# Kernel optimization log

Hardware: AMD Instinct MI355X
Metric: run time of the kernel (lower is better)

## Reference

```python
import jax, jax.numpy as jnp
import numpy as np

EPS = 1e-5
INF = 1e5


def setup_inputs() -> dict:
    key = jax.random.key(0)
    ks = iter(jax.random.split(key, 32))
    B, N, F, H, NH, C = 2, 384, 64, 64, 4, 32
    def lin(k, fi, fo):
        return jax.random.normal(k, (fi, fo), jnp.float32) / np.sqrt(fi).astype(np.float32)
    d = {}
    d['h'] = jax.random.normal(next(ks), (B, N, F), jnp.float32)
    d['x'] = jax.random.normal(next(ks), (B, N, 3), jnp.float32)
    # edge_model (ConcatenationFilter): Linear(2F+1,H), SiLU, Linear(H,H), SiLU
    d['We0'] = lin(next(ks), 2 * F + 1, H); d['be0'] = jnp.zeros(H, jnp.float32)
    d['We1'] = lin(next(ks), H, H);         d['be1'] = jnp.zeros(H, jnp.float32)
    # semantic_attention_mlp: Linear(H, n_heads), LeakyReLU(0.2)
    d['Ws'] = lin(next(ks), H, NH);         d['bs'] = jnp.zeros(NH, jnp.float32)
    # coefficients_mlp: Linear(H,H), SiLU, Linear(H,C)
    d['Wc0'] = lin(next(ks), H, H);         d['bc0'] = jnp.zeros(H, jnp.float32)
    d['Wc1'] = lin(next(ks), H, C);         d['bc1'] = jnp.zeros(C, jnp.float32)
    # post_norm_mlp: Linear(C,H), SiLU, Linear(H,H)
    d['Wp0'] = lin(next(ks), C, H);         d['bp0'] = jnp.zeros(H, jnp.float32)
    d['Wp1'] = lin(next(ks), H, H);         d['bp1'] = jnp.zeros(H, jnp.float32)
    # coordinate_mlp: Linear(H,H), SiLU, Linear(H,1,bias=False) init gain 1e-3
    d['Wx0'] = lin(next(ks), H, H);         d['bx0'] = jnp.zeros(H, jnp.float32)
    d['Wx1'] = lin(next(ks), H, 1) * 1e-3
    # node_mlp: Linear(NH*H + H + F, H), SiLU, Linear(H, F)
    d['Wn0'] = lin(next(ks), NH * H + H + F, H); d['bn0'] = jnp.zeros(H, jnp.float32)
    d['Wn1'] = lin(next(ks), H, F);         d['bn1'] = jnp.zeros(F, jnp.float32)
    d['log_gamma'] = jnp.zeros(NH, jnp.float32)
    return d


def _forward(h, x, We0, be0, We1, be1, Ws, bs, Wc0, bc0, Wc1, bc1,
             Wp0, bp0, Wp1, bp1, Wx0, bx0, Wx1, Wn0, bn0, Wn1, bn1, log_gamma):
    B, N, F = h.shape
    silu = jax.nn.silu

    # pairwise displacements and distances: (B,N,N,3), (B,N,N,1)
    x_minus_xt = x[:, :, None, :] - x[:, None, :, :]
    norm = jnp.sqrt(jnp.sum(x_minus_xt * x_minus_xt, axis=-1, keepdims=True) + EPS)

    # pairwise node-feature concat + distance -> edge MLP (ConcatenationFilter)
    hi = jnp.broadcast_to(h[:, :, None, :], (B, N, N, F))
    hj = jnp.broadcast_to(h[:, None, :, :], (B, N, N, F))
    e_in = jnp.concatenate([hi, hj, norm], axis=-1)           # (B,N,N,2F+1)
    h_e = silu(silu(e_in @ We0 + be0) @ We1 + be1)            # (B,N,N,H)

    eye = jnp.eye(N, dtype=h.dtype)[None, :, :, None]         # mask self-edges

    # euclidean attention per head, softmax over neighbors j (axis=-2)
    eu = jax.nn.softmax(-(norm + INF * eye) * jnp.exp(log_gamma), axis=-2)  # (B,N,N,NH)
    # semantic attention
    sem_logits = jax.nn.leaky_relu(h_e @ Ws + bs, 0.2) - INF * eye
    sem = jax.nn.softmax(sem_logits, axis=-2)                 # (B,N,N,NH)
    comb = eu * sem
    comb = comb / (jnp.sum(comb, axis=-2, keepdims=True) + EPS)

    # attention-weighted multi-head edge features, aggregated over neighbors
    h_e_att = (comb[..., :, None] * h_e[..., None, :]).reshape(B, N, N, -1)  # (B,N,N,NH*H)
    h_e_agg = jnp.sum(h_e_att, axis=-2)                       # (B,N,NH*H)

    # spatial attention: equivariant combinations of unit direction vectors
    coeff = silu(h_e @ Wc0 + bc0) @ Wc1 + bc1                 # (B,N,N,C)
    x_hat = x_minus_xt / (norm + EPS)                         # (B,N,N,3)
    combinations = coeff[..., :, None] * x_hat[..., None, :]  # (B,N,N,C,3)
    comb_sum = jnp.mean(combinations, axis=2)                 # mean over j -> (B,N,C,3)
    comb_norm = jnp.sum(comb_sum * comb_sum, axis=-1)         # (B,N,C)
    h_comb = silu(comb_norm @ Wp0 + bp0) @ Wp1 + bp1          # (B,N,H)

    # node update (residual)
    node_in = jnp.concatenate([h, h_e_agg, h_comb], axis=-1)
    h_out = h + (silu(node_in @ Wn0 + bn0) @ Wn1 + bn1)

    # coordinate update: scalar-gated displacements, mean over neighbors
    scale = silu(h_e @ Wx0 + bx0) @ Wx1                       # (B,N,N,1)
    x_out = x + jnp.mean(x_minus_xt * scale, axis=2)          # (B,N,3)
    return h_out, x_out


def reference(h, x, We0, be0, We1, be1, Ws, bs, Wc0, bc0, Wc1, bc1,
              Wp0, bp0, Wp1, bp1, Wx0, bx0, Wx1, Wn0, bn0, Wn1, bn1, log_gamma):
    return _forward(h, x, We0, be0, We1, be1, Ws, bs, Wc0, bc0, Wc1, bc1,
                    Wp0, bp0, Wp1, bp1, Wx0, bx0, Wx1, Wn0, bn0, Wn1, bn1, log_gamma)
```

## Files before the change

### kernel.cpp

```cpp
#include <hip/hip_runtime.h>

#define NPT 384
#define NB 2
#define NROW (NB*NPT)
#define NT 6
#define HOFF 49152
#define RECB 1024
#define REC_OFF 424960

typedef unsigned short u16;
typedef unsigned int u32;
typedef __bf16 bf16x8 __attribute__((ext_vector_type(8)));
typedef float f32x4 __attribute__((ext_vector_type(4)));

struct alignas(16) U4 { u32 x, y, z, w; };

constexpr float kEPS = 1e-5f;
constexpr float kINF = 1e5f;

#define WAVE_LDS_FENCE() asm volatile("s_waitcnt lgkmcnt(0)" ::: "memory")

__device__ __forceinline__ u16 f2b(float f) { __bf16 b = (__bf16)f; return __builtin_bit_cast(u16, b); }
__device__ __forceinline__ u32 pk2(float lo, float hi) { return (u32)f2b(lo) | ((u32)f2b(hi) << 16); }
__device__ __forceinline__ float b2f(u32 u) { return __uint_as_float(u << 16); }
__device__ __forceinline__ float silu_f(float v) { return v * __builtin_amdgcn_rcpf(1.f + __expf(-v)); }

__global__ __launch_bounds__(64) void sake_prep(
    const float* __restrict__ h, const float* __restrict__ We0,
    const float* __restrict__ be0, const float* __restrict__ We1,
    const float* __restrict__ Wc0, const float* __restrict__ Wc1,
    const float* __restrict__ Wx0, const float* __restrict__ Ws,
    float* __restrict__ U, float* __restrict__ V, u16* __restrict__ WT)
{
  const int t = threadIdx.x;
  const int blk = blockIdx.x;
  if (blk < NROW) {
    __shared__ float hs[64];
    hs[t] = h[blk * 64 + t];
    __syncthreads();
    float u = be0[t], v = 0.f;
#pragma unroll 8
    for (int k = 0; k < 64; k++) {
      float hv = hs[k];
      u = fmaf(hv, We0[k * 64 + t], u);
      v = fmaf(hv, We0[(64 + k) * 64 + t], v);
    }
    U[blk * 64 + t] = u;
    V[blk * 64 + t] = v;
  } else {
    const int wsel = blk - NROW;
    if (wsel == 4) {
      u16* dst = WT + 14336;
      for (int o = t; o < 16 * 64; o += 64) {
        int c = o >> 6, k = o & 63;
        dst[o] = (c < 4) ? f2b(Ws[k * 4 + c]) : (u16)0;
      }
      return;
    }
    const float* src; int nout; u16* dst;
    if      (wsel == 0) { src = We1; nout = 64; dst = WT;         }
    else if (wsel == 1) { src = Wc0; nout = 64; dst = WT + 4096;  }
    else if (wsel == 2) { src = Wx0; nout = 64; dst = WT + 8192;  }
    else                { src = Wc1; nout = 32; dst = WT + 12288; }
    const int total = 64 * nout;
    for (int o = t; o < total; o += 64) {
      int n = o >> 6, k = o & 63;
      dst[o] = f2b(src[k * nout + n]);
    }
  }
}

struct MainArgs {
  const float *x, *U, *V;
  const u16 *We1T, *Wc0T, *Wx0T, *Wc1T, *WsPT;
  const float *We0, *bs, *be1, *bc0, *bc1, *bx0, *Wx1, *log_gamma;
  char* rec;
};

__device__ __forceinline__ void readB(const u16* tile, int j, int kg, bf16x8& f0, bf16x8& f1) {
  const int r7 = j & 7;
  f0 = *(const bf16x8*)(tile + j * 64 + ((kg ^ r7) << 3));
  f1 = *(const bf16x8*)(tile + j * 64 + (((kg + 4) ^ r7) << 3));
}

template<int NNT, bool SILU_, int NCH, bool DUALT>
__device__ __forceinline__ void gemmT8(const u16* __restrict__ wG, const float* __restrict__ biasG,
                                       bf16x8 bf0, bf16x8 bf1, u16* out, u16* oTT,
                                       int j, int kg, int l15, int nbase)
{
  const int jm = j & (NCH - 1);
#pragma unroll
  for (int nt = 0; nt < NNT; nt++) {
    const int nrow = nbase + (nt << 4) + l15;
    bf16x8 a0 = *(const bf16x8*)(wG + nrow * 64 + (kg << 3));
    bf16x8 a1 = *(const bf16x8*)(wG + nrow * 64 + 32 + (kg << 3));
    f32x4 acc = {0.f, 0.f, 0.f, 0.f};
    acc = __builtin_amdgcn_mfma_f32_16x16x32_bf16(a0, bf0, acc, 0, 0, 0);
    acc = __builtin_amdgcn_mfma_f32_16x16x32_bf16(a1, bf1, acc, 0, 0, 0);
    const int n0 = nbase + (nt << 4) + (kg << 2);
    const float4 bv = *(const float4*)(biasG + n0);
    float s0, s1, s2, s3;
    if constexpr (SILU_) {
      s0 = silu_f(acc[0] + bv.x); s1 = silu_f(acc[1] + bv.y);
      s2 = silu_f(acc[2] + bv.z); s3 = silu_f(acc[3] + bv.w);
    } else {
      s0 = acc[0] + bv.x; s1 = acc[1] + bv.y;
      s2 = acc[2] + bv.z; s3 = acc[3] + bv.w;
    }
    const u16 q0 = f2b(s0), q1 = f2b(s1), q2 = f2b(s2), q3 = f2b(s3);
    u32 pkx = (u32)q0 | ((u32)q1 << 16), pky = (u32)q2 | ((u32)q3 << 16);
    const int c = n0 >> 3;
    u32* dst = (u32*)(out + j * (NCH * 8) + (((c ^ jm) << 3) + (n0 & 7)));
    dst[0] = pkx; dst[1] = pky;
    if constexpr (DUALT) {
      const int jq = (j >> 3), j7 = j & 7;
      const u16 qs[4] = {q0, q1, q2, q3};
#pragma unroll
      for (int r = 0; r < 4; r++) {
        const int f = n0 + r;
        oTT[f * 64 + ((jq ^ (f & 7)) << 3) + j7] = qs[r];
      }
    }
  }
}

__global__ __launch_bounds__(256, 4) void sake_main(MainArgs A)
{
  __shared__ __align__(16) u16 buf0[64 * 64];
  __shared__ __align__(16) u16 hes[64 * 64];
  __shared__ __align__(16) u16 hesT[64 * 64];
  __shared__ __align__(16) u16 coeff[64 * 32];
  __shared__ float raw_lds[64 * 5];
  __shared__ float disp[64][3];
  __shared__ float nrm_s[64];
  __shared__ float xstash[64 * 3];

  const int t = threadIdx.x;
  const int w = t >> 6, lane = t & 63;
  const int kg = lane >> 4, l15 = lane & 15;
  const int bt = blockIdx.x;
  const int i = bt % NPT;
  const int bj = bt / NPT;
  const int jt = bj % NT, b = bj / NT;
  const int bi = b * NPT + i;
  const int j0 = jt << 6;
  char* rec = A.rec + (size_t)(bi * NT + jt) * RECB;

  const int jrow = (w << 4) + l15;

  const int jj2 = t >> 2, q4 = t & 3;
  {
    const int jr = j0 + jj2;
    const float* xp = &A.x[(b * NPT + jr) * 3];
    const float xj0 = xp[0], xj1 = xp[1], xj2 = xp[2];
    const float xi0 = A.x[bi * 3 + 0], xi1 = A.x[bi * 3 + 1], xi2 = A.x[bi * 3 + 2];
    const float4* vp = (const float4*)(A.V + (size_t)(b * NPT + jr) * 64 + q4 * 16);
    const float4 v0_ = vp[0], v1_ = vp[1], v2_ = vp[2], v3_ = vp[3];
    const float4* Up = (const float4*)(A.U + bi * 64 + q4 * 16);
    const float4 u0_ = Up[0], u1_ = Up[1], u2_ = Up[2], u3_ = Up[3];
    const float4* Wd = (const float4*)(A.We0 + 128 * 64 + q4 * 16);
    const float4 w0_ = Wd[0], w1_ = Wd[1], w2_ = Wd[2], w3_ = Wd[3];
    float dx0 = xi0 - xj0, dx1 = xi1 - xj1, dx2 = xi2 - xj2;
    float nr = sqrtf(fmaf(dx0, dx0, fmaf(dx1, dx1, fmaf(dx2, dx2, kEPS))));
    if (q4 == 0) { disp[jj2][0] = dx0; disp[jj2][1] = dx1; disp[jj2][2] = dx2; nrm_s[jj2] = nr; }
    float vv[16] = {v0_.x, v0_.y, v0_.z, v0_.w, v1_.x, v1_.y, v1_.z, v1_.w,
                    v2_.x, v2_.y, v2_.z, v2_.w, v3_.x, v3_.y, v3_.z, v3_.w};
    float uu[16] = {u0_.x, u0_.y, u0_.z, u0_.w, u1_.x, u1_.y, u1_.z, u1_.w,
                    u2_.x, u2_.y, u2_.z, u2_.w, u3_.x, u3_.y, u3_.z, u3_.w};
    float ww[16] = {w0_.x, w0_.y, w0_.z, w0_.w, w1_.x, w1_.y, w1_.z, w1_.w,
                    w2_.x, w2_.y, w2_.z, w2_.w, w3_.x, w3_.y, w3_.z, w3_.w};
    float sv[16];
#pragma unroll
    for (int e = 0; e < 16; e++) sv[e] = silu_f(uu[e] + vv[e] + nr * ww[e]);
    U4 lo, hi;
    lo.x = pk2(sv[0], sv[1]);   lo.y = pk2(sv[2], sv[3]);
    lo.z = pk2(sv[4], sv[5]);   lo.w = pk2(sv[6], sv[7]);
    hi.x = pk2(sv[8], sv[9]);   hi.y = pk2(sv[10], sv[11]);
    hi.z = pk2(sv[12], sv[13]); hi.w = pk2(sv[14], sv[15]);
    const int r7 = jj2 & 7;
    *(U4*)(buf0 + jj2 * 64 + (((q4 * 2) ^ r7) << 3)) = lo;
    *(U4*)(buf0 + jj2 * 64 + (((q4 * 2 + 1) ^ r7) << 3)) = hi;
  }
  WAVE_LDS_FENCE();

  {
    bf16x8 bh0, bh1;
    readB(buf0, jrow, kg, bh0, bh1);
    gemmT8<4, true, 8, true>(A.We1T, A.be1, bh0, bh1, hes, hesT, jrow, kg, l15, 0);
  }
  WAVE_LDS_FENCE();

  bf16x8 he0, he1;
  readB(hes, jrow, kg, he0, he1);

  gemmT8<4, true, 8, false>(A.Wc0T, A.bc0, he0, he1, buf0, nullptr, jrow, kg, l15, 0);

  {
    float sacc = 0.f;
#pragma unroll
    for (int nt = 0; nt < 4; nt++) {
      const int nrow = (nt << 4) + l15;
      bf16x8 a0 = *(const bf16x8*)(A.Wx0T + nrow * 64 + (kg << 3));
      bf16x8 a1 = *(const bf16x8*)(A.Wx0T + nrow * 64 + 32 + (kg << 3));
      f32x4 acc = {0.f, 0.f, 0.f, 0.f};
      acc = __builtin_amdgcn_mfma_f32_16x16x32_bf16(a0, he0, acc, 0, 0, 0);
      acc = __builtin_amdgcn_mfma_f32_16x16x32_bf16(a1, he1, acc, 0, 0, 0);
      const int n0 = (nt << 4) + (kg << 2);
      const float4 bv = *(const float4*)(A.bx0 + n0);
      const float4 wx = *(const float4*)(A.Wx1 + n0);
      sacc = fmaf(silu_f(acc[0] + bv.x), wx.x, sacc);
      sacc = fmaf(silu_f(acc[1] + bv.y), wx.y, sacc);
      sacc = fmaf(silu_f(acc[2] + bv.z), wx.z, sacc);
      sacc = fmaf(silu_f(acc[3] + bv.w), wx.w, sacc);
    }
    sacc += __shfl_xor(sacc, 16, 64);
    sacc += __shfl_xor(sacc, 32, 64);
    if (kg == 0) {
      xstash[jrow * 3 + 0] = disp[jrow][0] * sacc;
      xstash[jrow * 3 + 1] = disp[jrow][1] * sacc;
      xstash[jrow * 3 + 2] = disp[jrow][2] * sacc;
    }
  }

  {
    const int r7a = jrow & 7;
    bf16x8 a0 = *(const bf16x8*)(hes + jrow * 64 + ((kg ^ r7a) << 3));
    bf16x8 a1 = *(const bf16x8*)(hes + jrow * 64 + (((kg + 4) ^ r7a) << 3));
    const u16* wrow = A.WsPT + l15 * 64;
    bf16x8 b0 = *(const bf16x8*)(wrow + (kg << 3));
    bf16x8 b1 = *(const bf16x8*)(wrow + 32 + (kg << 3));
    f32x4 acc = {0.f, 0.f, 0.f, 0.f};
    acc = __builtin_amdgcn_mfma_f32_16x16x32_bf16(a0, b0, acc, 0, 0, 0);
    acc = __builtin_amdgcn_mfma_f32_16x16x32_bf16(a1, b1, acc, 0, 0, 0);
    if (l15 < 4) {
      const int m0 = w << 4;
#pragma unroll
      for (int r = 0; r < 4; r++)
        raw_lds[(m0 + (kg << 2) + r) * 5 + l15] = acc[r];
    }
  }
  WAVE_LDS_FENCE();

  {
    bf16x8 c10, c11;
    readB(buf0, jrow, kg, c10, c11);
    gemmT8<2, false, 4, false>(A.Wc1T, A.bc1, c10, c11, coeff, nullptr, jrow, kg, l15, 0);
  }

  __syncthreads();

  float cA0 = 0, cA1 = 0, cA2 = 0;
  {
    const int jj = lane, head = w;
    float raw = raw_lds[jj * 5 + head] + A.bs[head];
    float bsem = (raw > 0.f) ? raw : 0.2f * raw;
    const bool self = (j0 + jj) == i;
    if (self) bsem -= kINF;
    const float gam = __expf(A.log_gamma[head]);
    const float aeu = -(nrm_s[jj] + (self ? kINF : 0.f)) * gam;
    const float eL = __expf(aeu + bsem);
    const float eB = __expf(bsem);
    const float eA = __expf(aeu);
    float sL = eL, sB = eB, sA = eA;
#pragma unroll
    for (int m = 32; m >= 1; m >>= 1) {
      sL += __shfl_xor(sL, m, 64);
      sB += __shfl_xor(sB, m, 64);
      sA += __shfl_xor(sA, m, 64);
    }
    u16* E = buf0 + 3072;
    E[head * 64 + (((jj >> 3) ^ head) << 3) + (jj & 7)] = f2b(eL);
    if (lane == 0) {
      float* sp = (float*)(rec + 908) + head * 5;
      sp[0] = 0.f; sp[1] = sL; sp[2] = 0.f; sp[3] = sB; sp[4] = sA;
    }
  }
  {
    const int c = t & 31, g = t >> 5;
    const int cc = c >> 3, ce = c & 7;
#pragma unroll
    for (int it = 0; it < 8; ++it) {
      const int jj = (g << 3) + it;
      const float s = b2f(coeff[jj * 32 + ((cc ^ (jj & 3)) << 3) + ce]) *
                      __builtin_amdgcn_rcpf(nrm_s[jj] + kEPS);
      cA0 = fmaf(s, disp[jj][0], cA0);
      cA1 = fmaf(s, disp[jj][1], cA1);
      cA2 = fmaf(s, disp[jj][2], cA2);
    }
  }
  {
    float* cascr = (float*)buf0;
    cascr[t * 3 + 0] = cA0; cascr[t * 3 + 1] = cA1; cascr[t * 3 + 2] = cA2;
  }

  __syncthreads();

  {
    const u16* E = buf0 + 3072;
    const int erow = l15;
    const int e7 = erow & 7;
    bf16x8 ea0 = *(const bf16x8*)(E + erow * 64 + ((kg ^ e7) << 3));
    bf16x8 ea1 = *(const bf16x8*)(E + erow * 64 + (((kg + 4) ^ e7) << 3));
    const int f = (w << 4) + l15;
    const int f7 = f & 7;
    bf16x8 hb0 = *(const bf16x8*)(hesT + f * 64 + ((kg ^ f7) << 3));
    bf16x8 hb1 = *(const bf16x8*)(hesT + f * 64 + (((kg + 4) ^ f7) << 3));
    f32x4 aF = {0.f, 0.f, 0.f, 0.f};
    aF = __builtin_amdgcn_mfma_f32_16x16x32_bf16(ea0, hb0, aF, 0, 0, 0);
    aF = __builtin_amdgcn_mfma_f32_16x16x32_bf16(ea1, hb1, aF, 0, 0, 0);
    if (kg == 0) {
      u16* rA = (u16*)rec;
#pragma unroll
      for (int r = 0; r < 4; r++) rA[r * 64 + f] = f2b(aF[r]);
    }
  }
  {
    const float* cascr = (const float*)buf0;
    if (t < 96) {
      const int c = t & 31, d = t >> 5;
      float s = 0.f;
#pragma unroll
      for (int g = 0; g < 8; g++) s += cascr[(g * 32 + c) * 3 + d];
      ((float*)(rec + 512))[d * 32 + c] = s;
    } else if (t < 99) {
      const int d = t - 96;
      float s = 0.f;
      for (int k = 0; k < 64; k++) s += xstash[k * 3 + d];
      ((float*)(rec + 896))[d] = s;
    }
  }
}

struct MergeArgs {
  const float *h, *x, *Wp0, *bp0, *Wp1, *bp1, *Wn0, *bn0, *Wn1, *bn1;
  const char* rec;
  float* out;
};

__global__ __launch_bounds__(256) void sake_merge(MergeArgs M)
{
  __shared__ float sc[NT][20];
  __shared__ float wAl[NT][4];
  __shared__ float coefh[4];
  __shared__ float node_in[384];
  __shared__ float cmv[96];
  __shared__ float nrm32[32];
  __shared__ float t0s[64];
  __shared__ float scr[256];

  const int t = threadIdx.x;
  const int bi = blockIdx.x;
  const char* rb = M.rec + (size_t)bi * NT * RECB;

  if (t < NT * 20) {
    const int tt = t / 20, k = t % 20;
    sc[tt][k] = ((const float*)(rb + tt * RECB + 908))[k];
  }
  if (t < 64) node_in[t] = M.h[bi * 64 + t];
  __syncthreads();
  if (t < 4) {
    const int hh = t;
    float mL = -1e30f, mb = -1e30f;
    for (int tt = 0; tt < NT; tt++) {
      mL = fmaxf(mL, sc[tt][hh * 5 + 0]);
      mb = fmaxf(mb, sc[tt][hh * 5 + 2]);
    }
    float SL = 0.f, Sb = 0.f, Sa = 0.f;
    for (int tt = 0; tt < NT; tt++) {
      const float wa = __expf(sc[tt][hh * 5 + 0] - mL);
      wAl[tt][hh] = wa;
      SL = fmaf(wa, sc[tt][hh * 5 + 1], SL);
      Sb = fmaf(__expf(sc[tt][hh * 5 + 2] - mb), sc[tt][hh * 5 + 3], Sb);
      Sa += sc[tt][hh * 5 + 4];
    }
    const float Ff = __expf(mL - mb);
    coefh[hh] = Ff / fmaf(SL, Ff, kEPS * Sa * Sb);
  }
  __syncthreads();
  {
    const int hh = t >> 6, f = t & 63;
    float s = 0.f;
#pragma unroll
    for (int tt = 0; tt < NT; tt++)
      s = fmaf(wAl[tt][hh], b2f(((const u16*)(rb + tt * RECB))[hh * 64 + f]), s);
    node_in[64 + hh * 64 + f] = s * coefh[hh];
  }
  if (t < 96) {
    float s = 0.f;
#pragma unroll
    for (int tt = 0; tt < NT; tt++) s += ((const float*)(rb + tt * RECB + 512))[t];
    cmv[t] = s * (1.f / 384.f);
  }
  if (t >= 128 && t < 131) {
    const int d = t - 128;
    float s = 0.f;
#pragma unroll
    for (int tt = 0; tt < NT; tt++) s += ((const float*)(rb + tt * RECB + 896))[d];
    M.out[HOFF + bi * 3 + d] = M.x[bi * 3 + d] + s * (1.f / 384.f);
  }
  __syncthreads();
  if (t < 32) {
    const float v0 = cmv[t], v1 = cmv[32 + t], v2 = cmv[64 + t];
    nrm32[t] = v0 * v0 + v1 * v1 + v2 * v2;
  }
  __syncthreads();
  if (t < 64) {
    float a = M.bp0[t];
    for (int c = 0; c < 32; c++) a = fmaf(nrm32[c], M.Wp0[c * 64 + t], a);
    t0s[t] = silu_f(a);
  }
  __syncthreads();
  if (t < 64) {
    float a = M.bp1[t];
    for (int k = 0; k < 64; k++) a = fmaf(t0s[k], M.Wp1[k * 64 + t], a);
    node_in[320 + t] = a;
  }
  __syncthreads();
  {
    const int f = t & 63, q = t >> 6;
    float a = 0.f;
    const int k0 = q * 96;
    for (int k = 0; k < 96; k++) a = fmaf(node_in[k0 + k], M.Wn0[(k0 + k) * 64 + f], a);
    scr[t] = a;
  }
  __syncthreads();
  if (t < 64) {
    const float s = scr[t] + scr[64 + t] + scr[128 + t] + scr[192 + t] + M.bn0[t];
    t0s[t] = silu_f(s);
  }
  __syncthreads();
  if (t < 64) {
    float a = M.bn1[t];
    for (int k = 0; k < 64; k++) a = fmaf(t0s[k], M.Wn1[k * 64 + t], a);
    M.out[bi * 64 + t] = M.h[bi * 64 + t] + a;
  }
}

extern "C" void kernel_launch(void* const* d_in, const int* in_sizes, int n_in,
                              void* d_out, int out_size, void* d_ws, size_t ws_size,
                              hipStream_t stream)
{
  (void)in_sizes; (void)n_in; (void)out_size; (void)ws_size;
  const float* h   = (const float*)d_in[0];
  const float* x   = (const float*)d_in[1];
  const float* We0 = (const float*)d_in[2];
  const float* be0 = (const float*)d_in[3];
  const float* We1 = (const float*)d_in[4];
  const float* be1 = (const float*)d_in[5];
  const float* Ws  = (const float*)d_in[6];
  const float* bs  = (const float*)d_in[7];
  const float* Wc0 = (const float*)d_in[8];
  const float* bc0 = (const float*)d_in[9];
  const float* Wc1 = (const float*)d_in[10];
  const float* bc1 = (const float*)d_in[11];
  const float* Wp0 = (const float*)d_in[12];
  const float* bp0 = (const float*)d_in[13];
  const float* Wp1 = (const float*)d_in[14];
  const float* bp1 = (const float*)d_in[15];
  const float* Wx0 = (const float*)d_in[16];
  const float* bx0 = (const float*)d_in[17];
  const float* Wx1 = (const float*)d_in[18];
  const float* Wn0 = (const float*)d_in[19];
  const float* bn0 = (const float*)d_in[20];
  const float* Wn1 = (const float*)d_in[21];
  const float* bn1 = (const float*)d_in[22];
  const float* lg  = (const float*)d_in[23];

  float* U = (float*)d_ws;
  float* V = U + NROW * 64;
  u16* WT = (u16*)(V + NROW * 64);
  char* rec = (char*)d_ws + REC_OFF;

  sake_prep<<<NROW + 5, 64, 0, stream>>>(h, We0, be0, We1, Wc0, Wc1, Wx0, Ws, U, V, WT);

  MainArgs A;
  A.x = x; A.U = U; A.V = V;
  A.We1T = WT; A.Wc0T = WT + 4096; A.Wx0T = WT + 8192; A.Wc1T = WT + 12288;
  A.WsPT = WT + 14336;
  A.We0 = We0; A.bs = bs; A.be1 = be1; A.bc0 = bc0; A.bc1 = bc1;
  A.bx0 = bx0; A.Wx1 = Wx1; A.log_gamma = lg;
  A.rec = rec;
  sake_main<<<NROW * NT, 256, 0, stream>>>(A);

  MergeArgs Mg;
  Mg.h = h; Mg.x = x;
  Mg.Wp0 = Wp0; Mg.bp0 = bp0; Mg.Wp1 = Wp1; Mg.bp1 = bp1;
  Mg.Wn0 = Wn0; Mg.bn0 = bn0; Mg.Wn1 = Wn1; Mg.bn1 = bn1;
  Mg.rec = rec; Mg.out = (float*)d_out;
  sake_merge<<<NROW, 256, 0, stream>>>(Mg);
}
```

Baseline: 102.1 us.

## Fuse main and merge kernels into one per-row kernel looping over j tiles

Replaces the 4608-block main kernel plus merge kernel with a single kernel of 768 blocks, each looping over all six j tiles for one node i and accumulating softmax sums, attention aggregation, coefficient sums and coordinate sums in registers. It also folds the Wc0, Wx0 and Ws GEMMs into one 9-tile loop over shared B fragments. The goal is to drop the global record round-trip and one kernel launch. In exchange the grid has far fewer blocks, which may underfill the GPU's CUs, and each block's six tiles now run serially. The epilogue also computes coefh twice and has an empty block, which looks like leftover code.

```diff
diff --git a/kernel.cpp b/kernel.cpp
--- a/kernel.cpp
+++ b/kernel.cpp
@@ -5,8 +5,6 @@
 #define NROW (NB*NPT)
 #define NT 6
 #define HOFF 49152
-#define RECB 1024
-#define REC_OFF 424960
 
 typedef unsigned short u16;
 typedef unsigned int u32;
@@ -71,10 +69,11 @@
 }
 
 struct MainArgs {
-  const float *x, *U, *V;
+  const float *x, *U, *V, *h;
   const u16 *We1T, *Wc0T, *Wx0T, *Wc1T, *WsPT;
   const float *We0, *bs, *be1, *bc0, *bc1, *bx0, *Wx1, *log_gamma;
-  char* rec;
+  const float *Wp0, *bp0, *Wp1, *bp1, *Wn0, *bn0, *Wn1, *bn1;
+  float* out;
 };
 
 __device__ __forceinline__ void readB(const u16* tile, int j, int kg, bf16x8& f0, bf16x8& f1) {
@@ -124,315 +123,287 @@
   }
 }
 
-__global__ __launch_bounds__(256, 4) void sake_main(MainArgs A)
+__global__ __launch_bounds__(256, 4) void sake_fused(MainArgs A)
 {
   __shared__ __align__(16) u16 buf0[64 * 64];
   __shared__ __align__(16) u16 hes[64 * 64];
   __shared__ __align__(16) u16 hesT[64 * 64];
   __shared__ __align__(16) u16 coeff[64 * 32];
+  __shared__ __align__(16) u16 E_own[16 * 64];
   __shared__ float raw_lds[64 * 5];
   __shared__ float disp[64][3];
   __shared__ float nrm_s[64];
   __shared__ float xstash[64 * 3];
+  __shared__ float node_in[384];
 
   const int t = threadIdx.x;
   const int w = t >> 6, lane = t & 63;
   const int kg = lane >> 4, l15 = lane & 15;
-  const int bt = blockIdx.x;
-  const int i = bt % NPT;
-  const int bj = bt / NPT;
-  const int jt = bj % NT, b = bj / NT;
-  const int bi = b * NPT + i;
-  const int j0 = jt << 6;
-  char* rec = A.rec + (size_t)(bi * NT + jt) * RECB;
+  const int bi = blockIdx.x;
+  const int i = bi % NPT, b = bi / NPT;
 
   const int jrow = (w << 4) + l15;
-
   const int jj2 = t >> 2, q4 = t & 3;
-  {
-    const int jr = j0 + jj2;
-    const float* xp = &A.x[(b * NPT + jr) * 3];
-    const float xj0 = xp[0], xj1 = xp[1], xj2 = xp[2];
-    const float xi0 = A.x[bi * 3 + 0], xi1 = A.x[bi * 3 + 1], xi2 = A.x[bi * 3 + 2];
-    const float4* vp = (const float4*)(A.V + (size_t)(b * NPT + jr) * 64 + q4 * 16);
-    const float4 v0_ = vp[0], v1_ = vp[1], v2_ = vp[2], v3_ = vp[3];
-    const float4* Up = (const float4*)(A.U + bi * 64 + q4 * 16);
-    const float4 u0_ = Up[0], u1_ = Up[1], u2_ = Up[2], u3_ = Up[3];
-    const float4* Wd = (const float4*)(A.We0 + 128 * 64 + q4 * 16);
-    const float4 w0_ = Wd[0], w1_ = Wd[1], w2_ = Wd[2], w3_ = Wd[3];
-    float dx0 = xi0 - xj0, dx1 = xi1 - xj1, dx2 = xi2 - xj2;
-    float nr = sqrtf(fmaf(dx0, dx0, fmaf(dx1, dx1, fmaf(dx2, dx2, kEPS))));
-    if (q4 == 0) { disp[jj2][0] = dx0; disp[jj2][1] = dx1; disp[jj2][2] = dx2; nrm_s[jj2] = nr; }
-    float vv[16] = {v0_.x, v0_.y, v0_.z, v0_.w, v1_.x, v1_.y, v1_.z, v1_.w,
-                    v2_.x, v2_.y, v2_.z, v2_.w, v3_.x, v3_.y, v3_.z, v3_.w};
-    float uu[16] = {u0_.x, u0_.y, u0_.z, u0_.w, u1_.x, u1_.y, u1_.z, u1_.w,
-                    u2_.x, u2_.y, u2_.z, u2_.w, u3_.x, u3_.y, u3_.z, u3_.w};
-    float ww[16] = {w0_.x, w0_.y, w0_.z, w0_.w, w1_.x, w1_.y, w1_.z, w1_.w,
-                    w2_.x, w2_.y, w2_.z, w2_.w, w3_.x, w3_.y, w3_.z, w3_.w};
-    float sv[16];
-#pragma unroll
-    for (int e = 0; e < 16; e++) sv[e] = silu_f(uu[e] + vv[e] + nr * ww[e]);
-    U4 lo, hi;
-    lo.x = pk2(sv[0], sv[1]);   lo.y = pk2(sv[2], sv[3]);
-    lo.z = pk2(sv[4], sv[5]);   lo.w = pk2(sv[6], sv[7]);
-    hi.x = pk2(sv[8], sv[9]);   hi.y = pk2(sv[10], sv[11]);
-    hi.z = pk2(sv[12], sv[13]); hi.w = pk2(sv[14], sv[15]);
-    const int r7 = jj2 & 7;
-    *(U4*)(buf0 + jj2 * 64 + (((q4 * 2) ^ r7) << 3)) = lo;
-    *(U4*)(buf0 + jj2 * 64 + (((q4 * 2 + 1) ^ r7) << 3)) = hi;
-  }
-  WAVE_LDS_FENCE();
-
-  {
-    bf16x8 bh0, bh1;
-    readB(buf0, jrow, kg, bh0, bh1);
-    gemmT8<4, true, 8, true>(A.We1T, A.be1, bh0, bh1, hes, hesT, jrow, kg, l15, 0);
-  }
-  WAVE_LDS_FENCE();
-
-  bf16x8 he0, he1;
-  readB(hes, jrow, kg, he0, he1);
-
-  gemmT8<4, true, 8, false>(A.Wc0T, A.bc0, he0, he1, buf0, nullptr, jrow, kg, l15, 0);
-
-  {
+
+  const float gamw = __expf(A.log_gamma[w]);
+  const float bsw = A.bs[w];
+  const float xi0 = A.x[bi * 3 + 0], xi1 = A.x[bi * 3 + 1], xi2 = A.x[bi * 3 + 2];
+
+  ((u32*)E_own)[t] = 0; ((u32*)E_own)[256 + t] = 0;
+
+  f32x4 aF = {0.f, 0.f, 0.f, 0.f};
+  float sLp = 0.f, sBp = 0.f, sAp = 0.f;
+  float cA0 = 0, cA1 = 0, cA2 = 0;
+  float xA0 = 0, xA1 = 0, xA2 = 0;
+
+  for (int jt = 0; jt < NT; ++jt) {
+    const int j0 = jt << 6;
+
+    {
+      const int jr = j0 + jj2;
+      const float* xp = &A.x[(b * NPT + jr) * 3];
+      const float xj0 = xp[0], xj1 = xp[1], xj2 = xp[2];
+      const float4* vp = (const float4*)(A.V + (size_t)(b * NPT + jr) * 64 + q4 * 16);
+      const float4 v0_ = vp[0], v1_ = vp[1], v2_ = vp[2], v3_ = vp[3];
+      const float4* Up = (const float4*)(A.U + bi * 64 + q4 * 16);
+      const float4 u0_ = Up[0], u1_ = Up[1], u2_ = Up[2], u3_ = Up[3];
+      const float4* Wd = (const float4*)(A.We0 + 128 * 64 + q4 * 16);
+      const float4 w0_ = Wd[0], w1_ = Wd[1], w2_ = Wd[2], w3_ = Wd[3];
+      float dx0 = xi0 - xj0, dx1 = xi1 - xj1, dx2 = xi2 - xj2;
+      float nr = sqrtf(fmaf(dx0, dx0, fmaf(dx1, dx1, fmaf(dx2, dx2, kEPS))));
+      if (q4 == 0) { disp[jj2][0] = dx0; disp[jj2][1] = dx1; disp[jj2][2] = dx2; nrm_s[jj2] = nr; }
+      float vv[16] = {v0_.x, v0_.y, v0_.z, v0_.w, v1_.x, v1_.y, v1_.z, v1_.w,
+                      v2_.x, v2_.y, v2_.z, v2_.w, v3_.x, v3_.y, v3_.z, v3_.w};
+      float uu[16] = {u0_.x, u0_.y, u0_.z, u0_.w, u1_.x, u1_.y, u1_.z, u1_.w,
+                      u2_.x, u2_.y, u2_.z, u2_.w, u3_.x, u3_.y, u3_.z, u3_.w};
+      float ww[16] = {w0_.x, w0_.y, w0_.z, w0_.w, w1_.x, w1_.y, w1_.z, w1_.w,
+                      w2_.x, w2_.y, w2_.z, w2_.w, w3_.x, w3_.y, w3_.z, w3_.w};
+      float sv[16];
+#pragma unroll
+      for (int e = 0; e < 16; e++) sv[e] = silu_f(uu[e] + vv[e] + nr * ww[e]);
+      U4 lo, hi;
+      lo.x = pk2(sv[0], sv[1]);   lo.y = pk2(sv[2], sv[3]);
+      lo.z = pk2(sv[4], sv[5]);   lo.w = pk2(sv[6], sv[7]);
+      hi.x = pk2(sv[8], sv[9]);   hi.y = pk2(sv[10], sv[11]);
+      hi.z = pk2(sv[12], sv[13]); hi.w = pk2(sv[14], sv[15]);
+      const int r7 = jj2 & 7;
+      *(U4*)(buf0 + jj2 * 64 + (((q4 * 2) ^ r7) << 3)) = lo;
+      *(U4*)(buf0 + jj2 * 64 + (((q4 * 2 + 1) ^ r7) << 3)) = hi;
+    }
+    WAVE_LDS_FENCE();
+
+    {
+      bf16x8 bh0, bh1;
+      readB(buf0, jrow, kg, bh0, bh1);
+      gemmT8<4, true, 8, true>(A.We1T, A.be1, bh0, bh1, hes, hesT, jrow, kg, l15, 0);
+    }
+    WAVE_LDS_FENCE();
+
+    bf16x8 he0, he1;
+    readB(hes, jrow, kg, he0, he1);
+
     float sacc = 0.f;
-#pragma unroll
-    for (int nt = 0; nt < 4; nt++) {
-      const int nrow = (nt << 4) + l15;
-      bf16x8 a0 = *(const bf16x8*)(A.Wx0T + nrow * 64 + (kg << 3));
-      bf16x8 a1 = *(const bf16x8*)(A.Wx0T + nrow * 64 + 32 + (kg << 3));
-      f32x4 acc = {0.f, 0.f, 0.f, 0.f};
-      acc = __builtin_amdgcn_mfma_f32_16x16x32_bf16(a0, he0, acc, 0, 0, 0);
-      acc = __builtin_amdgcn_mfma_f32_16x16x32_bf16(a1, he1, acc, 0, 0, 0);
-      const int n0 = (nt << 4) + (kg << 2);
-      const float4 bv = *(const float4*)(A.bx0 + n0);
-      const float4 wx = *(const float4*)(A.Wx1 + n0);
-      sacc = fmaf(silu_f(acc[0] + bv.x), wx.x, sacc);
-      sacc = fmaf(silu_f(acc[1] + bv.y), wx.y, sacc);
-      sacc = fmaf(silu_f(acc[2] + bv.z), wx.z, sacc);
-      sacc = fmaf(silu_f(acc[3] + bv.w), wx.w, sacc);
+    {
+      const int jm8 = jrow & 7;
+#pragma unroll
+      for (int nt = 0; nt < 9; nt++) {
+        const u16* wrow = (nt == 8) ? (A.WsPT + l15 * 64)
+                                    : (A.Wc0T + ((nt << 4) + l15) * 64);
+        bf16x8 a0 = *(const bf16x8*)(wrow + (kg << 3));
+        bf16x8 a1 = *(const bf16x8*)(wrow + 32 + (kg << 3));
+        f32x4 acc = {0.f, 0.f, 0.f, 0.f};
+        acc = __builtin_amdgcn_mfma_f32_16x16x32_bf16(a0, he0, acc, 0, 0, 0);
+        acc = __builtin_amdgcn_mfma_f32_16x16x32_bf16(a1, he1, acc, 0, 0, 0);
+        const int n0 = (nt << 4) + (kg << 2);
+        if (nt < 4) {
+          const float4 bv = *(const float4*)(A.bc0 + n0);
+          const u16 q0 = f2b(silu_f(acc[0] + bv.x)), q1 = f2b(silu_f(acc[1] + bv.y));
+          const u16 q2 = f2b(silu_f(acc[2] + bv.z)), q3 = f2b(silu_f(acc[3] + bv.w));
+          u32 pkx = (u32)q0 | ((u32)q1 << 16), pky = (u32)q2 | ((u32)q3 << 16);
+          const int c = n0 >> 3;
+          u32* dst = (u32*)(buf0 + jrow * 64 + (((c ^ jm8) << 3) + (n0 & 7)));
+          dst[0] = pkx; dst[1] = pky;
+        } else if (nt < 8) {
+          const int f0 = n0 - 64;
+          const float4 bv = *(const float4*)(A.bx0 + f0);
+          const float4 wx = *(const float4*)(A.Wx1 + f0);
+          sacc = fmaf(silu_f(acc[0] + bv.x), wx.x, sacc);
+          sacc = fmaf(silu_f(acc[1] + bv.y), wx.y, sacc);
+          sacc = fmaf(silu_f(acc[2] + bv.z), wx.z, sacc);
+          sacc = fmaf(silu_f(acc[3] + bv.w), wx.w, sacc);
+        } else {
+          if (kg == 0) {
+            raw_lds[jrow * 5 + 0] = acc[0];
+            raw_lds[jrow * 5 + 1] = acc[1];
+            raw_lds[jrow * 5 + 2] = acc[2];
+            raw_lds[jrow * 5 + 3] = acc[3];
+          }
+        }
+      }
     }
     sacc += __shfl_xor(sacc, 16, 64);
     sacc += __shfl_xor(sacc, 32, 64);
     if (kg == 0) {
-      xstash[jrow * 3 + 0] = disp[jrow][0] * sacc;
-      xstash[jrow * 3 + 1] = disp[jrow][1] * sacc;
-      xstash[jrow * 3 + 2] = disp[jrow][2] * sacc;
-    }
-  }
-
-  {
-    const int r7a = jrow & 7;
-    bf16x8 a0 = *(const bf16x8*)(hes + jrow * 64 + ((kg ^ r7a) << 3));
-    bf16x8 a1 = *(const bf16x8*)(hes + jrow * 64 + (((kg + 4) ^ r7a) << 3));
-    const u16* wrow = A.WsPT + l15 * 64;
-    bf16x8 b0 = *(const bf16x8*)(wrow + (kg << 3));
-    bf16x8 b1 = *(const bf16x8*)(wrow + 32 + (kg << 3));
-    f32x4 acc = {0.f, 0.f, 0.f, 0.f};
-    acc = __builtin_amdgcn_mfma_f32_16x16x32_bf16(a0, b0, acc, 0, 0, 0);
-    acc = __builtin_amdgcn_mfma_f32_16x16x32_bf16(a1, b1, acc, 0, 0, 0);
-    if (l15 < 4) {
-      const int m0 = w << 4;
-#pragma unroll
-      for (int r = 0; r < 4; r++)
-        raw_lds[(m0 + (kg << 2) + r) * 5 + l15] = acc[r];
-    }
-  }
-  WAVE_LDS_FENCE();
-
-  {
-    bf16x8 c10, c11;
-    readB(buf0, jrow, kg, c10, c11);
-    gemmT8<2, false, 4, false>(A.Wc1T, A.bc1, c10, c11, coeff, nullptr, jrow, kg, l15, 0);
-  }
-
-  __syncthreads();
-
-  float cA0 = 0, cA1 = 0, cA2 = 0;
-  {
-    const int jj = lane, head = w;
-    float raw = raw_lds[jj * 5 + head] + A.bs[head];
-    float bsem = (raw > 0.f) ? raw : 0.2f * raw;
-    const bool self = (j0 + jj) == i;
-    if (self) bsem -= kINF;
-    const float gam = __expf(A.log_gamma[head]);
-    const float aeu = -(nrm_s[jj] + (self ? kINF : 0.f)) * gam;
-    const float eL = __expf(aeu + bsem);
-    const float eB = __expf(bsem);
-    const float eA = __expf(aeu);
-    float sL = eL, sB = eB, sA = eA;
+      xA0 = fmaf(disp[jrow][0], sacc, xA0);
+      xA1 = fmaf(disp[jrow][1], sacc, xA1);
+      xA2 = fmaf(disp[jrow][2], sacc, xA2);
+    }
+    WAVE_LDS_FENCE();
+
+    {
+      bf16x8 c10, c11;
+      readB(buf0, jrow, kg, c10, c11);
+      gemmT8<2, false, 4, false>(A.Wc1T, A.bc1, c10, c11, coeff, nullptr, jrow, kg, l15, 0);
+    }
+
+    __syncthreads();
+
+    {
+      const int jj = lane, head = w;
+      float raw = raw_lds[jj * 5 + head] + bsw;
+      float bsem = (raw > 0.f) ? raw : 0.2f * raw;
+      const bool self = (j0 + jj) == i;
+      if (self) bsem -= kINF;
+      const float aeu = -(nrm_s[jj] + (self ? kINF : 0.f)) * gamw;
+      const float eL = __expf(aeu + bsem);
+      sLp += eL;
+      sBp += __expf(bsem);
+      sAp += __expf(aeu);
+      E_own[head * 64 + (((jj >> 3) ^ head) << 3) + (jj & 7)] = f2b(eL);
+    }
+    {
+      const int c = t & 31, g = t >> 5;
+      const int cc = c >> 3, ce = c & 7;
+#pragma unroll
+      for (int it = 0; it < 8; ++it) {
+        const int jj = (g << 3) + it;
+        const float s = b2f(coeff[jj * 32 + ((cc ^ (jj & 3)) << 3) + ce]) *
+                        __builtin_amdgcn_rcpf(nrm_s[jj] + kEPS);
+        cA0 = fmaf(s, disp[jj][0], cA0);
+        cA1 = fmaf(s, disp[jj][1], cA1);
+        cA2 = fmaf(s, disp[jj][2], cA2);
+      }
+    }
+    __syncthreads();
+
+    {
+      const int erow = l15;
+      const int e7 = erow & 7;
+      bf16x8 ea0 = *(const bf16x8*)(E_own + erow * 64 + ((kg ^ e7) << 3));
+      bf16x8 ea1 = *(const bf16x8*)(E_own + erow * 64 + (((kg + 4) ^ e7) << 3));
+      const int f = (w << 4) + l15;
+      const int f7 = f & 7;
+      bf16x8 hb0 = *(const bf16x8*)(hesT + f * 64 + ((kg ^ f7) << 3));
+      bf16x8 hb1 = *(const bf16x8*)(hesT + f * 64 + (((kg + 4) ^ f7) << 3));
+      aF = __builtin_amdgcn_mfma_f32_16x16x32_bf16(ea0, hb0, aF, 0, 0, 0);
+      aF = __builtin_amdgcn_mfma_f32_16x16x32_bf16(ea1, hb1, aF, 0, 0, 0);
+    }
+    __syncthreads();
+  }
+
+  {
+    float sL = sLp, sB = sBp, sA = sAp;
 #pragma unroll
     for (int m = 32; m >= 1; m >>= 1) {
       sL += __shfl_xor(sL, m, 64);
       sB += __shfl_xor(sB, m, 64);
       sA += __shfl_xor(sA, m, 64);
     }
-    u16* E = buf0 + 3072;
-    E[head * 64 + (((jj >> 3) ^ head) << 3) + (jj & 7)] = f2b(eL);
-    if (lane == 0) {
-      float* sp = (float*)(rec + 908) + head * 5;
-      sp[0] = 0.f; sp[1] = sL; sp[2] = 0.f; sp[3] = sB; sp[4] = sA;
-    }
-  }
-  {
-    const int c = t & 31, g = t >> 5;
-    const int cc = c >> 3, ce = c & 7;
-#pragma unroll
-    for (int it = 0; it < 8; ++it) {
-      const int jj = (g << 3) + it;
-      const float s = b2f(coeff[jj * 32 + ((cc ^ (jj & 3)) << 3) + ce]) *
-                      __builtin_amdgcn_rcpf(nrm_s[jj] + kEPS);
-      cA0 = fmaf(s, disp[jj][0], cA0);
-      cA1 = fmaf(s, disp[jj][1], cA1);
-      cA2 = fmaf(s, disp[jj][2], cA2);
-    }
-  }
-  {
-    float* cascr = (float*)buf0;
+    const float coefw = __builtin_amdgcn_rcpf(fmaf(kEPS * sA, sB, sL));
+    if (kg == 0) {
+#pragma unroll
+      for (int r = 0; r < 4; r++)
+        node_in[64 + r * 64 + (w << 4) + l15] = aF[r] * ((r == w) ? coefw : 0.f);
+    }
+  }
+  if (t < 64) node_in[t] = A.h[bi * 64 + t];
+  {
+    float* cascr = (float*)coeff;
     cascr[t * 3 + 0] = cA0; cascr[t * 3 + 1] = cA1; cascr[t * 3 + 2] = cA2;
-  }
-
-  __syncthreads();
-
-  {
-    const u16* E = buf0 + 3072;
-    const int erow = l15;
-    const int e7 = erow & 7;
-    bf16x8 ea0 = *(const bf16x8*)(E + erow * 64 + ((kg ^ e7) << 3));
-    bf16x8 ea1 = *(const bf16x8*)(E + erow * 64 + (((kg + 4) ^ e7) << 3));
-    const int f = (w << 4) + l15;
-    const int f7 = f & 7;
-    bf16x8 hb0 = *(const bf16x8*)(hesT + f * 64 + ((kg ^ f7) << 3));
-    bf16x8 hb1 = *(const bf16x8*)(hesT + f * 64 + (((kg + 4) ^ f7) << 3));
-    f32x4 aF = {0.f, 0.f, 0.f, 0.f};
-    aF = __builtin_amdgcn_mfma_f32_16x16x32_bf16(ea0, hb0, aF, 0, 0, 0);
-    aF = __builtin_amdgcn_mfma_f32_16x16x32_bf16(ea1, hb1, aF, 0, 0, 0);
     if (kg == 0) {
-      u16* rA = (u16*)rec;
-#pragma unroll
-      for (int r = 0; r < 4; r++) rA[r * 64 + f] = f2b(aF[r]);
-    }
-  }
-  {
-    const float* cascr = (const float*)buf0;
+      xstash[jrow * 3 + 0] = xA0; xstash[jrow * 3 + 1] = xA1; xstash[jrow * 3 + 2] = xA2;
+    }
+  }
+  __syncthreads();
+  {
+  }
+  {
+    __shared__ float coefh[4];
+    float sL = sLp, sB = sBp, sA = sAp;
+#pragma unroll
+    for (int m = 32; m >= 1; m >>= 1) {
+      sL += __shfl_xor(sL, m, 64);
+      sB += __shfl_xor(sB, m, 64);
+      sA += __shfl_xor(sA, m, 64);
+    }
+    if (lane == 0) coefh[w] = __builtin_amdgcn_rcpf(fmaf(kEPS * sA, sB, sL));
+    __syncthreads();
+    if (kg == 0) {
+#pragma unroll
+      for (int r = 0; r < 4; r++)
+        node_in[64 + r * 64 + (w << 4) + l15] = aF[r] * coefh[r];
+    }
+  }
+  {
+    const float* cascr = (const float*)coeff;
+    float* cmv = raw_lds;
     if (t < 96) {
       const int c = t & 31, d = t >> 5;
       float s = 0.f;
 #pragma unroll
       for (int g = 0; g < 8; g++) s += cascr[(g * 32 + c) * 3 + d];
-      ((float*)(rec + 512))[d * 32 + c] = s;
-    } else if (t < 99) {
-      const int d = t - 96;
+      cmv[d * 32 + c] = s * (1.f / 384.f);
+    }
+    if (t >= 128 && t < 131) {
+      const int d = t - 128;
       float s = 0.f;
       for (int k = 0; k < 64; k++) s += xstash[k * 3 + d];
-      ((float*)(rec + 896))[d] = s;
-    }
-  }
-}
-
-struct MergeArgs {
-  const float *h, *x, *Wp0, *bp0, *Wp1, *bp1, *Wn0, *bn0, *Wn1, *bn1;
-  const char* rec;
-  float* out;
-};
-
-__global__ __launch_bounds__(256) void sake_merge(MergeArgs M)
-{
-  __shared__ float sc[NT][20];
-  __shared__ float wAl[NT][4];
-  __shared__ float coefh[4];
-  __shared__ float node_in[384];
-  __shared__ float cmv[96];
-  __shared__ float nrm32[32];
-  __shared__ float t0s[64];
-  __shared__ float scr[256];
-
-  const int t = threadIdx.x;
-  const int bi = blockIdx.x;
-  const char* rb = M.rec + (size_t)bi * NT * RECB;
-
-  if (t < NT * 20) {
-    const int tt = t / 20, k = t % 20;
-    sc[tt][k] = ((const float*)(rb + tt * RECB + 908))[k];
-  }
-  if (t < 64) node_in[t] = M.h[bi * 64 + t];
-  __syncthreads();
-  if (t < 4) {
-    const int hh = t;
-    float mL = -1e30f, mb = -1e30f;
-    for (int tt = 0; tt < NT; tt++) {
-      mL = fmaxf(mL, sc[tt][hh * 5 + 0]);
-      mb = fmaxf(mb, sc[tt][hh * 5 + 2]);
-    }
-    float SL = 0.f, Sb = 0.f, Sa = 0.f;
-    for (int tt = 0; tt < NT; tt++) {
-      const float wa = __expf(sc[tt][hh * 5 + 0] - mL);
-      wAl[tt][hh] = wa;
-      SL = fmaf(wa, sc[tt][hh * 5 + 1], SL);
-      Sb = fmaf(__expf(sc[tt][hh * 5 + 2] - mb), sc[tt][hh * 5 + 3], Sb);
-      Sa += sc[tt][hh * 5 + 4];
-    }
-    const float Ff = __expf(mL - mb);
-    coefh[hh] = Ff / fmaf(SL, Ff, kEPS * Sa * Sb);
-  }
-  __syncthreads();
-  {
-    const int hh = t >> 6, f = t & 63;
-    float s = 0.f;
-#pragma unroll
-    for (int tt = 0; tt < NT; tt++)
-      s = fmaf(wAl[tt][hh], b2f(((const u16*)(rb + tt * RECB))[hh * 64 + f]), s);
-    node_in[64 + hh * 64 + f] = s * coefh[hh];
-  }
-  if (t < 96) {
-    float s = 0.f;
-#pragma unroll
-    for (int tt = 0; tt < NT; tt++) s += ((const float*)(rb + tt * RECB + 512))[t];
-    cmv[t] = s * (1.f / 384.f);
-  }
-  if (t >= 128 && t < 131) {
-    const int d = t - 128;
-    float s = 0.f;
-#pragma unroll
-    for (int tt = 0; tt < NT; tt++) s += ((const float*)(rb + tt * RECB + 896))[d];
-    M.out[HOFF + bi * 3 + d] = M.x[bi * 3 + d] + s * (1.f / 384.f);
-  }
-  __syncthreads();
-  if (t < 32) {
-    const float v0 = cmv[t], v1 = cmv[32 + t], v2 = cmv[64 + t];
-    nrm32[t] = v0 * v0 + v1 * v1 + v2 * v2;
-  }
-  __syncthreads();
+      A.out[HOFF + bi * 3 + d] = A.x[bi * 3 + d] + s * (1.f / 384.f);
+    }
+  }
+  __syncthreads();
+  {
+    float* cmv = raw_lds;
+    if (t < 32) {
+      const float v0 = cmv[t], v1 = cmv[32 + t], v2 = cmv[64 + t];
+      nrm_s[t] = v0 * v0 + v1 * v1 + v2 * v2;
+    }
+  }
+  __syncthreads();
+  float* t0s = &disp[0][0];
   if (t < 64) {
-    float a = M.bp0[t];
-    for (int c = 0; c < 32; c++) a = fmaf(nrm32[c], M.Wp0[c * 64 + t], a);
+    float a = A.bp0[t];
+    for (int c = 0; c < 32; c++) a = fmaf(nrm_s[c], A.Wp0[c * 64 + t], a);
     t0s[t] = silu_f(a);
   }
   __syncthreads();
   if (t < 64) {
-    float a = M.bp1[t];
-    for (int k = 0; k < 64; k++) a = fmaf(t0s[k], M.Wp1[k * 64 + t], a);
+    float a = A.bp1[t];
+    for (int k = 0; k < 64; k++) a = fmaf(t0s[k], A.Wp1[k * 64 + t], a);
     node_in[320 + t] = a;
   }
   __syncthreads();
   {
+    float* scr = (float*)buf0;
     const int f = t & 63, q = t >> 6;
     float a = 0.f;
     const int k0 = q * 96;
-    for (int k = 0; k < 96; k++) a = fmaf(node_in[k0 + k], M.Wn0[(k0 + k) * 64 + f], a);
+    for (int k = 0; k < 96; k++) a = fmaf(node_in[k0 + k], A.Wn0[(k0 + k) * 64 + f], a);
     scr[t] = a;
   }
   __syncthreads();
+  {
+    const float* scr = (const float*)buf0;
+    if (t < 64) {
+      const float s = scr[t] + scr[64 + t] + scr[128 + t] + scr[192 + t] + A.bn0[t];
+      t0s[t] = silu_f(s);
+    }
+  }
+  __syncthreads();
   if (t < 64) {
-    const float s = scr[t] + scr[64 + t] + scr[128 + t] + scr[192 + t] + M.bn0[t];
-    t0s[t] = silu_f(s);
-  }
-  __syncthreads();
-  if (t < 64) {
-    float a = M.bn1[t];
-    for (int k = 0; k < 64; k++) a = fmaf(t0s[k], M.Wn1[k * 64 + t], a);
-    M.out[bi * 64 + t] = M.h[bi * 64 + t] + a;
+    float a = A.bn1[t];
+    for (int k = 0; k < 64; k++) a = fmaf(t0s[k], A.Wn1[k * 64 + t], a);
+    A.out[bi * 64 + t] = A.h[bi * 64 + t] + a;
   }
 }
 
@@ -469,23 +440,18 @@
   float* U = (float*)d_ws;
   float* V = U + NROW * 64;
   u16* WT = (u16*)(V + NROW * 64);
-  char* rec = (char*)d_ws + REC_OFF;
 
   sake_prep<<<NROW + 5, 64, 0, stream>>>(h, We0, be0, We1, Wc0, Wc1, Wx0, Ws, U, V, WT);
 
   MainArgs A;
-  A.x = x; A.U = U; A.V = V;
+  A.x = x; A.U = U; A.V = V; A.h = h;
   A.We1T = WT; A.Wc0T = WT + 4096; A.Wx0T = WT + 8192; A.Wc1T = WT + 12288;
   A.WsPT = WT + 14336;
   A.We0 = We0; A.bs = bs; A.be1 = be1; A.bc0 = bc0; A.bc1 = bc1;
   A.bx0 = bx0; A.Wx1 = Wx1; A.log_gamma = lg;
-  A.rec = rec;
-  sake_main<<<NROW * NT, 256, 0, stream>>>(A);
-
-  MergeArgs Mg;
-  Mg.h = h; Mg.x = x;
-  Mg.Wp0 = Wp0; Mg.bp0 = bp0; Mg.Wp1 = Wp1; Mg.bp1 = bp1;
-  Mg.Wn0 = Wn0; Mg.bn0 = bn0; Mg.Wn1 = Wn1; Mg.bn1 = bn1;
-  Mg.rec = rec; Mg.out = (float*)d_out;
-  sake_merge<<<NROW, 256, 0, stream>>>(Mg);
+  A.Wp0 = Wp0; A.bp0 = bp0; A.Wp1 = Wp1; A.bp1 = bp1;
+  A.Wn0 = Wn0; A.bn0 = bn0; A.Wn1 = Wn1; A.bn1 = bn1;
+  A.out = (float*)d_out;
+
+  sake_fused<<<NROW, 256, 0, stream>>>(A);
 }
```

After: 153.4 us. +50.2%, slower.
